# Kernel tuning notes

Hardware: AMD Instinct MI355X
Metric: run time of the kernel (lower is better)

The kernel has to match this reference:

```python
import jax, jax.numpy as jnp
import numpy as np

HIDDEN = 2560
NUM_HEADS = 80
HEAD_DIM = 64
STATE = 128
N_GROUPS = 1
CONV_K = 4
CHUNK = 256
INTER = 2 * HIDDEN                       # 5120 = NUM_HEADS * HEAD_DIM
CONV_DIM = INTER + 2 * N_GROUPS * STATE  # 5376
PROJ = INTER + CONV_DIM + NUM_HEADS      # 10576
EPS = 1e-5
DT_MIN, DT_MAX = 0.0, 100.0


def segment_sum(x):
    # x: (..., T) -> (..., T, T); out[i, j] = sum_{j < k <= i} x[k], -inf above diag
    T = x.shape[-1]
    xe = jnp.broadcast_to(x[..., :, None], x.shape + (T,))  # [i, j] = x[i]
    mask_lo = jnp.tril(jnp.ones((T, T), dtype=bool), -1)
    seg = jnp.cumsum(jnp.where(mask_lo, xe, 0.0), axis=-2)
    mask = jnp.tril(jnp.ones((T, T), dtype=bool), 0)
    return jnp.where(mask, seg, -jnp.inf)


def setup_inputs() -> dict:
    key = jax.random.key(0)
    k0, k1, k2, k3 = jax.random.split(key, 4)
    x = jax.random.normal(k0, (2, 2048, HIDDEN), jnp.float32)
    in_proj_w = jax.random.normal(k1, (PROJ, HIDDEN), jnp.float32) * (HIDDEN ** -0.5)
    conv1d_w = jax.random.normal(k2, (CONV_DIM, CONV_K), jnp.float32) * (CONV_K ** -0.5)
    conv1d_b = jnp.zeros((CONV_DIM,), jnp.float32)
    A_log = jnp.log(jnp.arange(1, NUM_HEADS + 1, dtype=jnp.float32))
    D = jnp.ones((NUM_HEADS,), jnp.float32)
    dt_bias = jnp.ones((NUM_HEADS,), jnp.float32)
    norm_weight = jnp.ones((INTER,), jnp.float32)
    out_proj_w = jax.random.normal(k3, (HIDDEN, INTER), jnp.float32) * (INTER ** -0.5)
    return dict(input_states=x, in_proj_w=in_proj_w, conv1d_w=conv1d_w,
                conv1d_b=conv1d_b, A_log=A_log, D=D, dt_bias=dt_bias,
                norm_weight=norm_weight, out_proj_w=out_proj_w)


def _mamba2_forward(input_states, in_proj_w, conv1d_w, conv1d_b, A_log, D,
                    dt_bias, norm_weight, out_proj_w):
    b, s, _ = input_states.shape
    proj = input_states @ in_proj_w.T                       # (b, s, PROJ)
    gate, hs, dt = jnp.split(proj, [INTER, INTER + CONV_DIM], axis=-1)

    # causal depthwise conv1d + SiLU
    xT = jnp.transpose(hs, (0, 2, 1))                       # (b, conv_dim, s)
    xT = jnp.pad(xT, ((0, 0), (0, 0), (CONV_K - 1, 0)))
    conv = jax.lax.conv_general_dilated(
        xT, conv1d_w[:, None, :], (1,), 'VALID',
        feature_group_count=CONV_DIM, dimension_numbers=('NCH', 'OIH', 'NCH'))
    hs = jax.nn.silu(jnp.transpose(conv + conv1d_b[None, :, None], (0, 2, 1)))

    hs, B, C = jnp.split(hs, [INTER, INTER + N_GROUPS * STATE], axis=-1)
    A = -jnp.exp(A_log)                                     # (h,)
    dt = jnp.clip(jax.nn.softplus(dt + dt_bias), DT_MIN, DT_MAX)  # (b, s, h)

    X = hs.reshape(b, s, NUM_HEADS, HEAD_DIM)
    rep = NUM_HEADS // N_GROUPS
    B = jnp.repeat(B.reshape(b, s, N_GROUPS, STATE), rep, axis=2)
    C = jnp.repeat(C.reshape(b, s, N_GROUPS, STATE), rep, axis=2)

    pad = (-s) % CHUNK
    D_res = D[None, None, :, None] * jnp.pad(X, ((0, 0), (0, pad), (0, 0), (0, 0)))
    Xd = X * dt[..., None]                                  # discretized input
    dA = A[None, None, :] * dt                              # (b, s, h)

    def chunk(t):
        t = jnp.pad(t, [(0, 0), (0, pad)] + [(0, 0)] * (t.ndim - 2))
        return t.reshape(t.shape[0], -1, CHUNK, *t.shape[2:])

    Xc, Bc, Cc = chunk(Xd), chunk(B), chunk(C)              # (b, c, l, h, ...)
    Ac = jnp.transpose(chunk(dA), (0, 3, 1, 2))             # (b, h, c, l)
    A_cum = jnp.cumsum(Ac, axis=-1)

    # 1. intra-chunk (diagonal block) outputs
    L = jnp.exp(segment_sum(Ac))                            # (b, h, c, l, l)
    G = jnp.einsum('bclhn,bcshn->bhcls', Cc, Bc)
    Y_diag = jnp.einsum('bhcls,bcshp->bclhp', G * L, Xc)

    # 2. per-chunk final states
    decay_states = jnp.exp(A_cum[..., -1:] - A_cum)         # (b, h, c, l)
    states = jnp.einsum('bclhn,bhcl,bclhp->bchpn', Bc, decay_states, Xc)

    # 3. inter-chunk recurrence
    A_last = A_cum[..., -1]                                 # (b, h, c)
    decay_chunk = jnp.exp(segment_sum(jnp.pad(A_last, ((0, 0), (0, 0), (1, 0)))))
    states = jnp.concatenate([jnp.zeros_like(states[:, :1]), states], axis=1)
    new_states = jnp.einsum('bhzc,bchpn->bzhpn', decay_chunk, states)
    states = new_states[:, :-1]                             # (b, c, h, p, n)

    # 4. state -> output conversion
    Y_off = jnp.einsum('bclhn,bchpn,bhcl->bclhp', Cc, states, jnp.exp(A_cum))

    y = (Y_diag + Y_off).reshape(b, -1, NUM_HEADS, HEAD_DIM) + D_res
    y = y[:, :s].reshape(b, s, INTER)

    # gated RMSNorm
    y = y * jax.nn.silu(gate)
    var = jnp.mean(y * y, axis=-1, keepdims=True)
    y = y * jax.lax.rsqrt(var + EPS) * norm_weight
    return y @ out_proj_w.T


def reference(input_states, in_proj_w, conv1d_w, conv1d_b, A_log, D, dt_bias,
              norm_weight, out_proj_w):
    return _mamba2_forward(input_states, in_proj_w, conv1d_w, conv1d_b, A_log,
                           D, dt_bias, norm_weight, out_proj_w)
```

## Files before the change

kernel.cpp:

```cpp
#include <hip/hip_runtime.h>
#include <hip/hip_bf16.h>
#include <math.h>

#define HIDDEN   2560
#define NUM_HEADS 80
#define HEAD_DIM 64
#define STATE    128
#define CONV_K   4
#define CHUNK    256
#define INTER    (2*HIDDEN)
#define CONV_DIM (INTER + 2*STATE)
#define PROJ     (INTER + CONV_DIM + NUM_HEADS)
#define PROJ_PAD 10624
#define NBC      336
#define EPS      1e-5f

#define BATCH 2
#define SEQ   2048
#define TOK   (BATCH*SEQ)
#define NC    (SEQ/CHUNK)
#define KSPLIT 16
#define KCH   (HIDDEN/KSPLIT)

typedef __attribute__((ext_vector_type(8))) short bf16x8;
typedef __attribute__((ext_vector_type(4))) float f32x4;

#define MFMA16(a,b,c) __builtin_amdgcn_mfma_f32_16x16x32_bf16((a),(b),(c),0,0,0)

__device__ __forceinline__ unsigned short f2bf(float f){
    union{float f;unsigned u;}v; v.f=f;
    unsigned r = v.u + 0x7fffu + ((v.u>>16)&1u);
    return (unsigned short)(r>>16);
}
__device__ __forceinline__ float bf2f(unsigned short s){
    union{unsigned u;float f;}v; v.u = ((unsigned)s)<<16; return v.f;
}
__device__ __forceinline__ void unpack8(uint4 u, float* e){
    e[0]=bf2f((unsigned short)(u.x&0xffff)); e[1]=bf2f((unsigned short)(u.x>>16));
    e[2]=bf2f((unsigned short)(u.y&0xffff)); e[3]=bf2f((unsigned short)(u.y>>16));
    e[4]=bf2f((unsigned short)(u.z&0xffff)); e[5]=bf2f((unsigned short)(u.z>>16));
    e[6]=bf2f((unsigned short)(u.w&0xffff)); e[7]=bf2f((unsigned short)(u.w>>16));
}

__device__ __forceinline__ void gld16(const void* g, void* l){
    __builtin_amdgcn_global_load_lds((const __attribute__((address_space(1))) void*)g,
                                     (__attribute__((address_space(3))) void*)l, 16, 0, 0);
}

template<bool BF16OUT>
__global__ __launch_bounds__(256) void gemm_bf16(const unsigned short* __restrict__ A, int lda,
                                                 const unsigned short* __restrict__ B, int ldb,
                                                 void* __restrict__ Cv, int ldc, int K) {
    __shared__ unsigned short As[128][64];
    __shared__ unsigned short Bs[128][64];
    int tid = threadIdx.x;
    int lane = tid & 63, wid = tid >> 6;
    int wr = wid >> 1, wc = wid & 1;

    int bm, bn;
    if ((gridDim.y & 7) == 0) {
        int bid   = blockIdx.y * gridDim.x + blockIdx.x;
        int xcd   = bid & 7;
        int local = bid >> 3;
        int mrows = gridDim.y >> 3;
        bm = (xcd * mrows + (local % mrows)) * 128;
        bn = (local / mrows) * 128;
    } else {
        bm = blockIdx.y * 128;
        bn = blockIdx.x * 128;
    }

    f32x4 acc[4][4];
    #pragma unroll
    for (int i=0;i<4;i++)
        #pragma unroll
        for (int j=0;j<4;j++) acc[i][j] = (f32x4){0.f,0.f,0.f,0.f};

    int srow_off = lane >> 3;
    int sslot    = lane & 7;

    for (int k0 = 0; k0 < K; k0 += 64) {
        #pragma unroll
        for (int q=0;q<4;q++){
            int brow = (wid*4+q)*8;
            int row  = brow + srow_off;
            int sl   = sslot ^ (row & 7);
            gld16(A + (size_t)(bm + row)*lda + k0 + sl*8, &As[brow][0]);
            gld16(B + (size_t)(bn + row)*ldb + k0 + sl*8, &Bs[brow][0]);
        }
        __syncthreads();
        #pragma unroll
        for (int kk=0; kk<64; kk+=32){
            bf16x8 a[4], b[4];
            #pragma unroll
            for (int i=0;i<4;i++){
                int row = wr*64 + i*16 + (lane&15);
                int slot = ((kk>>3) + (lane>>4)) ^ (row & 7);
                a[i] = *(const bf16x8*)&As[row][slot*8];
            }
            #pragma unroll
            for (int j=0;j<4;j++){
                int row = wc*64 + j*16 + (lane&15);
                int slot = ((kk>>3) + (lane>>4)) ^ (row & 7);
                b[j] = *(const bf16x8*)&Bs[row][slot*8];
            }
            #pragma unroll
            for (int i=0;i<4;i++)
                #pragma unroll
                for (int j=0;j<4;j++)
                    acc[i][j] = MFMA16(a[i], b[j], acc[i][j]);
        }
        __syncthreads();
    }
    #pragma unroll
    for (int i=0;i<4;i++){
        int row0 = bm + wr*64 + i*16 + (lane>>4)*4;
        #pragma unroll
        for (int j=0;j<4;j++){
            int col = bn + wc*64 + j*16 + (lane&15);
            #pragma unroll
            for (int r=0;r<4;r++){
                if (BF16OUT)
                    ((unsigned short*)Cv)[(size_t)(row0+r)*ldc + col] = f2bf(acc[i][j][r]);
                else
                    ((float*)Cv)[(size_t)(row0+r)*ldc + col] = acc[i][j][r];
            }
        }
    }
}

__global__ __launch_bounds__(256) void cvt_bf16(const float* __restrict__ in,
                                                unsigned short* __restrict__ out, size_t n4){
    size_t i4 = (size_t)blockIdx.x*256 + threadIdx.x;
    if (i4 >= n4) return;
    size_t i = i4*4;
    float4 v = *(const float4*)(in+i);
    ushort4 o; o.x=f2bf(v.x); o.y=f2bf(v.y); o.z=f2bf(v.z); o.w=f2bf(v.w);
    *(ushort4*)(out+i) = o;
}
__global__ __launch_bounds__(256) void cvt_w1(const float* __restrict__ in,
                                              unsigned short* __restrict__ out){
    size_t i4 = (size_t)blockIdx.x*256 + threadIdx.x;
    if (i4 >= (size_t)PROJ_PAD*HIDDEN/4) return;
    size_t i = i4*4;
    int row = (int)(i / HIDDEN);
    ushort4 o;
    if (row < PROJ){
        float4 v = *(const float4*)(in+i);
        o.x=f2bf(v.x); o.y=f2bf(v.y); o.z=f2bf(v.z); o.w=f2bf(v.w);
    } else { o.x=o.y=o.z=o.w=0; }
    *(ushort4*)(out+i) = o;
}

#define BM 128
#define BN 128
#define BKK 16
__global__ __launch_bounds__(256) void gemm_bc_splitk(const float* __restrict__ A, int lda,
                                                      const float* __restrict__ B, int ldb,
                                                      float* __restrict__ Cpart) {
    __shared__ float As[BKK][BM];
    __shared__ float Bs[BKK][BN];
    int tid = threadIdx.x;
    int bm = blockIdx.y * BM, bn = blockIdx.x * BN;
    int z  = blockIdx.z;
    int ty = tid >> 4, tx = tid & 15;
    float acc[8][8];
    #pragma unroll
    for (int i=0;i<8;i++)
        #pragma unroll
        for (int j=0;j<8;j++) acc[i][j]=0.f;
    int lr = tid >> 1, lk = (tid & 1) * 8;
    for (int k0 = z*KCH; k0 < (z+1)*KCH; k0 += BKK) {
        #pragma unroll
        for (int u=0;u<8;u++)
            As[lk+u][lr] = A[(size_t)(bm+lr)*lda + k0 + lk + u];
        int ncol = bn + lr;
        if (ncol < NBC) {
            #pragma unroll
            for (int u=0;u<8;u++)
                Bs[lk+u][lr] = B[(size_t)ncol*ldb + k0 + lk + u];
        } else {
            #pragma unroll
            for (int u=0;u<8;u++) Bs[lk+u][lr] = 0.f;
        }
        __syncthreads();
        #pragma unroll
        for (int k=0;k<BKK;k++){
            float a[8], bb[8];
            #pragma unroll
            for (int i=0;i<8;i++) a[i] = As[k][ty*8+i];
            #pragma unroll
            for (int j=0;j<8;j++) bb[j] = Bs[k][tx*8+j];
            #pragma unroll
            for (int i=0;i<8;i++)
                #pragma unroll
                for (int j=0;j<8;j++) acc[i][j] += a[i]*bb[j];
        }
        __syncthreads();
    }
    float* Cz = Cpart + (size_t)z*TOK*NBC;
    #pragma unroll
    for (int i=0;i<8;i++){
        int m = bm + ty*8 + i;
        #pragma unroll
        for (int j=0;j<8;j++){
            int n = bn + tx*8 + j;
            if (n < NBC) Cz[(size_t)m*NBC + n] = acc[i][j];
        }
    }
}

__global__ __launch_bounds__(256) void reduce_bc(const float* __restrict__ part,
                                                 const float* __restrict__ dt_bias,
                                                 float* __restrict__ outBC,
                                                 float* __restrict__ dtbuf) {
    size_t i4 = (size_t)blockIdx.x*256 + threadIdx.x;
    if (i4 >= (size_t)TOK*NBC/4) return;
    size_t i = i4*4;
    float4 s = *(const float4*)(part + i);
    #pragma unroll
    for (int z=1; z<KSPLIT; z++){
        float4 v = *(const float4*)(part + (size_t)z*TOK*NBC + i);
        s.x += v.x; s.y += v.y; s.z += v.z; s.w += v.w;
    }
    int col = (int)(i % NBC);
    int t   = (int)(i / NBC);
    if (col < 256) {
        *(float4*)(outBC + i) = s;
    } else {
        int h = col - 256;
        float e[4] = {s.x, s.y, s.z, s.w};
        #pragma unroll
        for (int u=0;u<4;u++){
            float xv = e[u] + dt_bias[h+u];
            float sp = (xv > 20.f) ? xv : log1pf(expf(xv));
            e[u] = fminf(fmaxf(sp, 0.f), 100.f);
        }
        float4 o; o.x=e[0]; o.y=e[1]; o.z=e[2]; o.w=e[3];
        *(float4*)(dtbuf + (size_t)t*NUM_HEADS + h) = o;
    }
}

__global__ __launch_bounds__(256) void conv_xt_kernel(const unsigned short* __restrict__ projb,
                                                      const float* __restrict__ cw,
                                                      const float* __restrict__ cb,
                                                      unsigned short* __restrict__ XT) {
    int t0 = blockIdx.x * 64;
    int d0 = blockIdx.y * 64;
    int b  = t0 / SEQ;
    int s0 = t0 % SEQ;
    __shared__ unsigned short raw[68][66];
    int tid = threadIdx.x;
    for (int f = tid; f < 67*8; f += 256){
        int r = f >> 3, g = f & 7;
        int sp = s0 - 3 + r;
        uint4 v;
        if (sp >= 0) v = *(const uint4*)(projb + ((size_t)(b*SEQ+sp))*PROJ_PAD + INTER + d0 + g*8);
        else { v.x=0u; v.y=0u; v.z=0u; v.w=0u; }
        unsigned int* dst = (unsigned int*)&raw[r][g*8];
        dst[0]=v.x; dst[1]=v.y; dst[2]=v.z; dst[3]=v.w;
    }
    __syncthreads();
    int t = tid & 63, dg = tid >> 6;
    #pragma unroll
    for (int dd = 0; dd < 16; dd++){
        int d = dg*16 + dd;
        float acc = cb[d0+d];
        #pragma unroll
        for (int j=0;j<CONV_K;j++)
            acc += cw[(d0+d)*CONV_K+j] * bf2f(raw[t+j][d]);
        float val = acc/(1.f+expf(-acc));
        XT[((size_t)(b*INTER + d0 + d))*SEQ + s0 + t] = f2bf(val);
    }
}

__global__ __launch_bounds__(256) void conv_bc_kernel(const float* __restrict__ projBC,
                                                      const float* __restrict__ cw,
                                                      const float* __restrict__ cb,
                                                      float* __restrict__ xBC_BC,
                                                      unsigned short* __restrict__ BT) {
    int idx = blockIdx.x*256 + threadIdx.x;
    if (idx >= TOK*256) return;
    int d = idx & 255;
    int t = idx >> 8;
    int b = t / SEQ, sl = t % SEQ;
    int dc = INTER + d;
    float acc = cb[dc];
    #pragma unroll
    for (int j=0;j<CONV_K;j++){
        int sp = sl - (CONV_K-1) + j;
        if (sp >= 0)
            acc += cw[dc*CONV_K+j] * projBC[((size_t)(b*SEQ+sp))*NBC + d];
    }
    float val = acc / (1.f + expf(-acc));
    xBC_BC[(size_t)t*256 + d] = val;
    if (d < 128)
        BT[((size_t)(b*128 + d))*SEQ + sl] = f2bf(val);
}

__global__ __launch_bounds__(256) void cumsum_kernel(const float* __restrict__ dtbuf,
                                                     const float* __restrict__ A_log,
                                                     float* __restrict__ A_cum) {
    int c = blockIdx.x, h = blockIdx.y, b = blockIdx.z;
    int l = threadIdx.x;
    float A = -expf(A_log[h]);
    float v = A * dtbuf[(size_t)(b*SEQ + c*CHUNK + l)*NUM_HEADS + h];
    __shared__ float buf[CHUNK];
    buf[l] = v;
    __syncthreads();
    for (int off=1; off<CHUNK; off<<=1){
        float t = (l>=off) ? buf[l-off] : 0.f;
        __syncthreads();
        buf[l] += t;
        __syncthreads();
    }
    A_cum[((size_t)b*NUM_HEADS + h)*SEQ + c*CHUNK + l] = buf[l];
}

__global__ __launch_bounds__(256) void g_kernel(const float* __restrict__ xBC_BC,
                                                unsigned short* __restrict__ G) {
    int p = blockIdx.x, c = blockIdx.y, b = blockIdx.z;
    int lt = 0, a0 = 0;
    while (a0 + lt + 1 <= p) { a0 += lt + 1; lt++; }
    int st = p - a0;
    int l0 = lt*64, s0 = st*64;
    __shared__ float Cs[64][68];
    __shared__ float Bs[64][68];
    int tid = threadIdx.x, ty = tid >> 4, tx = tid & 15;
    float acc[4][4];
    #pragma unroll
    for (int i=0;i<4;i++)
        #pragma unroll
        for (int j=0;j<4;j++) acc[i][j]=0.f;

    size_t rowC = ((size_t)(b*SEQ + c*CHUNK + l0))*256 + 128;
    size_t rowB = ((size_t)(b*SEQ + c*CHUNK + s0))*256;
    for (int kc=0; kc<2; kc++){
        #pragma unroll
        for (int it=0; it<4; it++){
            int f = tid + it*256;
            int r = f >> 4, c4 = f & 15;
            float4 cv = *(const float4*)(xBC_BC + rowC + (size_t)r*256 + kc*64 + c4*4);
            float4 bv = *(const float4*)(xBC_BC + rowB + (size_t)r*256 + kc*64 + c4*4);
            *(float4*)&Cs[r][c4*4] = cv;
            *(float4*)&Bs[r][c4*4] = bv;
        }
        __syncthreads();
        #pragma unroll 8
        for (int k=0;k<64;k++){
            float a[4], bb[4];
            #pragma unroll
            for (int i=0;i<4;i++) a[i] = Cs[ty*4+i][k];
            #pragma unroll
            for (int j=0;j<4;j++) bb[j] = Bs[tx*4+j][k];
            #pragma unroll
            for (int i=0;i<4;i++)
                #pragma unroll
                for (int j=0;j<4;j++) acc[i][j] += a[i]*bb[j];
        }
        __syncthreads();
    }
    size_t Gb = ((size_t)(b*NC + c)) << 16;
    #pragma unroll
    for (int i=0;i<4;i++){
        ushort4 g4;
        g4.x = f2bf(acc[i][0]); g4.y = f2bf(acc[i][1]);
        g4.z = f2bf(acc[i][2]); g4.w = f2bf(acc[i][3]);
        *(ushort4*)(G + Gb + (size_t)(l0 + ty*4 + i)*256 + s0 + tx*4) = g4;
    }
}

__global__ __launch_bounds__(256) void states_mfma(const unsigned short* __restrict__ XT,
                                                   const unsigned short* __restrict__ BT,
                                                   const float* __restrict__ dtbuf,
                                                   const float* __restrict__ A_cum,
                                                   float* __restrict__ statesT) {
    int c = blockIdx.x, h = blockIdx.y, b = blockIdx.z;
    __shared__ unsigned short Asx[64][64];
    __shared__ unsigned short Bsw[128][64];
    __shared__ float wl[CHUNK];
    int tid = threadIdx.x, lane = tid & 63, wid = tid >> 6;
    {
        const float* ac = A_cum + ((size_t)(b*NUM_HEADS+h))*SEQ + c*CHUNK;
        float Alast = ac[CHUNK-1];
        wl[tid] = expf(Alast - ac[tid]) * dtbuf[((size_t)(b*SEQ + c*CHUNK + tid))*NUM_HEADS + h];
    }
    __syncthreads();
    f32x4 acc[4][2];
    #pragma unroll
    for (int i=0;i<4;i++)
        #pragma unroll
        for (int j=0;j<2;j++) acc[i][j] = (f32x4){0.f,0.f,0.f,0.f};

    for (int kc = 0; kc < 4; kc++){
        int lbase = kc*64;
        #pragma unroll
        for (int q=0;q<2;q++){
            int brow = (wid*2+q)*8;
            int row  = brow + (lane>>3);
            int sl   = (lane&7) ^ (row & 7);
            gld16(XT + ((size_t)(b*INTER + h*HEAD_DIM + row))*SEQ + c*CHUNK + lbase + sl*8,
                  &Asx[brow][0]);
        }
        #pragma unroll
        for (int it=0; it<4; it++){
            int f = tid + it*256;
            int r = f >> 3, g = f & 7;
            uint4 v = *(const uint4*)(BT + ((size_t)(b*128 + r))*SEQ + c*CHUNK + lbase + g*8);
            float e[8]; unpack8(v, e);
            unsigned short o[8];
            #pragma unroll
            for (int u=0;u<8;u++) o[u] = f2bf(e[u] * wl[lbase + g*8 + u]);
            int slot = g ^ (r & 7);
            *(ushort4*)&Bsw[r][slot*8]   = *(ushort4*)&o[0];
            *(ushort4*)&Bsw[r][slot*8+4] = *(ushort4*)&o[4];
        }
        __syncthreads();
        #pragma unroll
        for (int kk=0; kk<64; kk+=32){
            bf16x8 a[4], bb[2];
            #pragma unroll
            for (int i=0;i<4;i++){
                int row = i*16 + (lane&15);
                int slot = ((kk>>3)+(lane>>4)) ^ (row&7);
                a[i] = *(const bf16x8*)&Asx[row][slot*8];
            }
            #pragma unroll
            for (int j=0;j<2;j++){
                int row = wid*32 + j*16 + (lane&15);
                int slot = ((kk>>3)+(lane>>4)) ^ (row&7);
                bb[j] = *(const bf16x8*)&Bsw[row][slot*8];
            }
            #pragma unroll
            for (int i=0;i<4;i++)
                #pragma unroll
                for (int j=0;j<2;j++)
                    acc[i][j] = MFMA16(a[i], bb[j], acc[i][j]);
        }
        __syncthreads();
    }
    size_t sb = ((size_t)((b*NC + c)*NUM_HEADS + h))*(HEAD_DIM*STATE);
    #pragma unroll
    for (int i=0;i<4;i++){
        #pragma unroll
        for (int j=0;j<2;j++){
            int n = wid*32 + j*16 + (lane&15);
            int p0 = i*16 + (lane>>4)*4;
            #pragma unroll
            for (int r=0;r<4;r++)
                statesT[sb + (size_t)(p0+r)*128 + n] = acc[i][j][r];
        }
    }
}

__global__ __launch_bounds__(256) void recur_kernel(const float* __restrict__ A_cum,
                                                    float* __restrict__ states) {
    int h = blockIdx.x, b = blockIdx.y;
    int tid = threadIdx.x;
    float Srun[32];
    #pragma unroll
    for (int i=0;i<32;i++) Srun[i]=0.f;
    const float* acum = A_cum + ((size_t)b*NUM_HEADS + h)*SEQ;
    for (int c=0;c<NC;c++){
        float alast = acum[c*CHUNK + CHUNK-1];
        float dec = expf(alast);
        size_t base = ((size_t)((b*NC + c)*NUM_HEADS + h))*(HEAD_DIM*STATE);
        #pragma unroll
        for (int i=0;i<32;i++){
            size_t idx = base + (size_t)tid + (size_t)i*256;
            float raw = states[idx];
            states[idx] = Srun[i];
            Srun[i] = Srun[i]*dec + raw;
        }
    }
}

__global__ __launch_bounds__(256) void yscan_mfma(const unsigned short* __restrict__ G,
                                                  const float* __restrict__ xBC_BC,
                                                  const unsigned short* __restrict__ XT,
                                                  const float* __restrict__ dtbuf,
                                                  const float* __restrict__ A_cum,
                                                  const float* __restrict__ statesT,
                                                  const float* __restrict__ Dvec,
                                                  unsigned short* __restrict__ projb) {
    int xb = blockIdx.x;
    int c = xb >> 2, lt = xb & 3;
    int h = blockIdx.y, b = blockIdx.z;
    int l0 = lt*64;
    __shared__ __align__(16) char pool[32768];
    unsigned short (*Cs)[128] = (unsigned short(*)[128])pool;
    unsigned short (*St)[128] = (unsigned short(*)[128])(pool + 16384);
    unsigned short (*Gw)[64]  = (unsigned short(*)[64])pool;
    unsigned short (*Xs)[64]  = (unsigned short(*)[64])(pool + 8192);
    float (*Ot)[68]           = (float(*)[68])pool;
    __shared__ float ac[CHUNK], dts[CHUNK];
    int tid = threadIdx.x, lane = tid & 63, wid = tid >> 6;
    ac[tid]  = A_cum[((size_t)(b*NUM_HEADS + h))*SEQ + c*CHUNK + tid];
    dts[tid] = dtbuf[((size_t)(b*SEQ + c*CHUNK + tid))*NUM_HEADS + h];
    __syncthreads();

    size_t stb = ((size_t)((b*NC + c)*NUM_HEADS + h))*(HEAD_DIM*STATE);
    #pragma unroll
    for (int it=0; it<8; it++){
        int f = tid + it*256;
        int r = f >> 5, c4 = f & 31;
        float4 v = *(const float4*)(xBC_BC + ((size_t)(b*SEQ + c*CHUNK + l0 + r))*256 + 128 + c4*4);
        unsigned short o[4] = {f2bf(v.x),f2bf(v.y),f2bf(v.z),f2bf(v.w)};
        int col = c4*4;
        int slot = (col>>3) ^ (r&7);
        *(ushort4*)&Cs[r][slot*8 + (col&7)] = *(ushort4*)o;
        float4 w = *(const float4*)(statesT + stb + (size_t)r*128 + c4*4);
        unsigned short o2[4] = {f2bf(w.x),f2bf(w.y),f2bf(w.z),f2bf(w.w)};
        *(ushort4*)&St[r][slot*8 + (col&7)] = *(ushort4*)o2;
    }
    __syncthreads();

    f32x4 acc1[4];
    #pragma unroll
    for (int j=0;j<4;j++) acc1[j] = (f32x4){0.f,0.f,0.f,0.f};
    #pragma unroll
    for (int kk=0; kk<128; kk+=32){
        int arow = wid*16 + (lane&15);
        int aslot = ((kk>>3)+(lane>>4)) ^ (arow&7);
        bf16x8 a = *(const bf16x8*)&Cs[arow][aslot*8];
        #pragma unroll
        for (int j=0;j<4;j++){
            int brow = j*16 + (lane&15);
            int bslot = ((kk>>3)+(lane>>4)) ^ (brow&7);
            bf16x8 bb = *(const bf16x8*)&St[brow][bslot*8];
            acc1[j] = MFMA16(a, bb, acc1[j]);
        }
    }
    float el[4];
    #pragma unroll
    for (int r=0;r<4;r++) el[r] = expf(ac[l0 + wid*16 + (lane>>4)*4 + r]);
    float master[4][4];
    #pragma unroll
    for (int j=0;j<4;j++)
        #pragma unroll
        for (int r=0;r<4;r++) master[j][r] = acc1[j][r]*el[r];
    __syncthreads();

    size_t Gb = ((size_t)(b*NC + c)) << 16;
    f32x4 acc2[4];
    #pragma unroll
    for (int j=0;j<4;j++) acc2[j] = (f32x4){0.f,0.f,0.f,0.f};
    for (int st=0; st<=lt; st++){
        int s0 = st*64;
        #pragma unroll
        for (int it=0; it<2; it++){
            int f = tid + it*256;
            int r = f >> 3, g = f & 7;
            uint4 v = *(const uint4*)(G + Gb + (size_t)(l0 + r)*256 + s0 + g*8);
            float e[8]; unpack8(v, e);
            float acl = ac[l0 + r];
            unsigned short o[8];
            #pragma unroll
            for (int u=0;u<8;u++){
                int s = s0 + g*8 + u;
                float w = (s <= l0 + r) ? expf(acl - ac[s])*dts[s] : 0.f;
                o[u] = f2bf(e[u]*w);
            }
            int slot = g ^ (r&7);
            *(ushort4*)&Gw[r][slot*8]   = *(ushort4*)&o[0];
            *(ushort4*)&Gw[r][slot*8+4] = *(ushort4*)&o[4];
        }
        #pragma unroll
        for (int q=0;q<2;q++){
            int brow = (wid*2+q)*8;
            int row  = brow + (lane>>3);
            int sl   = (lane&7) ^ (row&7);
            gld16(XT + ((size_t)(b*INTER + h*HEAD_DIM + row))*SEQ + c*CHUNK + s0 + sl*8,
                  &Xs[brow][0]);
        }
        __syncthreads();
        #pragma unroll
        for (int kk=0; kk<64; kk+=32){
            int arow = wid*16 + (lane&15);
            int aslot = ((kk>>3)+(lane>>4)) ^ (arow&7);
            bf16x8 a = *(const bf16x8*)&Gw[arow][aslot*8];
            #pragma unroll
            for (int j=0;j<4;j++){
                int brow = j*16 + (lane&15);
                int bslot = ((kk>>3)+(lane>>4)) ^ (brow&7);
                bf16x8 bb = *(const bf16x8*)&Xs[brow][bslot*8];
                acc2[j] = MFMA16(a, bb, acc2[j]);
            }
        }
        if (st < lt) __syncthreads();
    }

    float Dh = Dvec[h];
    #pragma unroll
    for (int j=0;j<4;j++){
        int p = j*16 + (lane&15);
        #pragma unroll
        for (int r=0;r<4;r++){
            int sl_ = wid*16 + (lane>>4)*4 + r;
            int slot = (sl_>>3) ^ (p&7);
            float xv = bf2f(Xs[p][slot*8 + (sl_&7)]);
            master[j][r] += acc2[j][r] + Dh*xv;
        }
    }
    __syncthreads();

    #pragma unroll
    for (int j=0;j<4;j++){
        int p = j*16 + (lane&15);
        #pragma unroll
        for (int r=0;r<4;r++)
            Ot[wid*16 + (lane>>4)*4 + r][p] = master[j][r];
    }
    __syncthreads();
    #pragma unroll
    for (int it=0; it<4; it++){
        int f = tid + it*256;
        int r = f >> 4, c4 = f & 15;
        ushort4 o;
        o.x = f2bf(Ot[r][c4*4+0]); o.y = f2bf(Ot[r][c4*4+1]);
        o.z = f2bf(Ot[r][c4*4+2]); o.w = f2bf(Ot[r][c4*4+3]);
        *(ushort4*)(projb + ((size_t)(b*SEQ + c*CHUNK + l0 + r))*PROJ_PAD + INTER + h*HEAD_DIM + c4*4) = o;
    }
}

__global__ __launch_bounds__(256) void gate_norm_kernel(const unsigned short* __restrict__ projb,
                                                        const float* __restrict__ normw,
                                                        unsigned short* __restrict__ yb) {
    int t = blockIdx.x;
    int tid = threadIdx.x;
    const unsigned short* row = projb + (size_t)t*PROJ_PAD;
    __shared__ float red[4];
    float vals[20];
    float ss = 0.f;
    #pragma unroll
    for (int i=0;i<5;i++){
        int j = (tid + i*256)*4;
        ushort4 g4 = *(const ushort4*)(row + j);
        ushort4 y4 = *(const ushort4*)(row + INTER + j);
        #pragma unroll
        for (int u=0;u<4;u++){
            float g = bf2f(((const unsigned short*)&g4)[u]);
            float y = bf2f(((const unsigned short*)&y4)[u]);
            float gv = g / (1.f + expf(-g));
            float v = y * gv;
            vals[i*4+u] = v;
            ss += v*v;
        }
    }
    #pragma unroll
    for (int off=32; off; off>>=1) ss += __shfl_xor(ss, off);
    if ((tid&63)==0) red[tid>>6] = ss;
    __syncthreads();
    float tot = red[0]+red[1]+red[2]+red[3];
    float inv = rsqrtf(tot/(float)INTER + EPS);
    #pragma unroll
    for (int i=0;i<5;i++){
        int j = (tid + i*256)*4;
        ushort4 o;
        o.x = f2bf(vals[i*4+0] * inv * normw[j+0]);
        o.y = f2bf(vals[i*4+1] * inv * normw[j+1]);
        o.z = f2bf(vals[i*4+2] * inv * normw[j+2]);
        o.w = f2bf(vals[i*4+3] * inv * normw[j+3]);
        *(ushort4*)(yb + (size_t)t*INTER + j) = o;
    }
}

extern "C" void kernel_launch(void* const* d_in, const int* in_sizes, int n_in,
                              void* d_out, int out_size, void* d_ws, size_t ws_size,
                              hipStream_t stream) {
    const float* x        = (const float*)d_in[0];
    const float* in_w     = (const float*)d_in[1];
    const float* conv_w   = (const float*)d_in[2];
    const float* conv_b   = (const float*)d_in[3];
    const float* A_log    = (const float*)d_in[4];
    const float* Dvec     = (const float*)d_in[5];
    const float* dt_bias  = (const float*)d_in[6];
    const float* norm_w   = (const float*)d_in[7];
    const float* out_w    = (const float*)d_in[8];
    float* out = (float*)d_out;
    (void)ws_size; (void)n_in; (void)in_sizes; (void)out_size;

    const size_t PROJB   = (size_t)TOK*PROJ_PAD*2;
    const size_t PROJBCB = (size_t)TOK*NBC*4;
    const size_t XTB     = (size_t)TOK*INTER*2;
    const size_t XBCBCB  = (size_t)TOK*256*4;
    const size_t BTB     = (size_t)BATCH*128*SEQ*2;
    const size_t GBYTES  = (size_t)BATCH*NC*CHUNK*CHUNK*2;
    const size_t DTB     = (size_t)TOK*NUM_HEADS*4;
    const size_t ACUMB   = DTB;
    const size_t STB     = (size_t)BATCH*NC*NUM_HEADS*HEAD_DIM*STATE*4;
    const size_t XB      = (size_t)TOK*HIDDEN*2;
    const size_t YB      = (size_t)TOK*INTER*2;

    char* base = (char*)d_ws;
    size_t off = 0;
    unsigned short* projb  = (unsigned short*)(base + off); off += PROJB;
    float* projBC          = (float*)(base + off);          off += PROJBCB;
    unsigned short* XTp    = (unsigned short*)(base + off); off += XTB;
    float* xBC_BC          = (float*)(base + off);          off += XBCBCB;
    unsigned short* BTp    = (unsigned short*)(base + off); off += BTB;
    unsigned short* Gp     = (unsigned short*)(base + off); off += GBYTES;
    float* dtbuf           = (float*)(base + off);          off += DTB;
    float* A_cum           = (float*)(base + off);          off += ACUMB;
    float* statesT         = (float*)(base + off);          off += STB;
    char*  T               = base + off;
    unsigned short* xb  = (unsigned short*)T;
    unsigned short* w1b = (unsigned short*)(T + XB);
    float* bcpart       = (float*)T;
    unsigned short* yb  = (unsigned short*)T;
    unsigned short* w2b = (unsigned short*)(T + YB);

    const size_t XB_E = (size_t)TOK*HIDDEN;
    const size_t W1_E = (size_t)PROJ_PAD*HIDDEN;
    const size_t W2_E = (size_t)HIDDEN*INTER;

    cvt_bf16<<<(unsigned)((XB_E/4+255)/256), 256, 0, stream>>>(x, xb, XB_E/4);
    cvt_w1<<<(unsigned)((W1_E/4+255)/256), 256, 0, stream>>>(in_w, w1b);

    gemm_bf16<true><<<dim3(PROJ_PAD/128, TOK/128), 256, 0, stream>>>(xb, HIDDEN, w1b, HIDDEN,
                                                                     projb, PROJ_PAD, HIDDEN);
    gemm_bc_splitk<<<dim3((NBC+BN-1)/BN, TOK/BM, KSPLIT), 256, 0, stream>>>(
        x, HIDDEN, in_w + (size_t)(INTER+INTER)*HIDDEN, HIDDEN, bcpart);
    reduce_bc<<<(unsigned)(((size_t)TOK*NBC/4+255)/256), 256, 0, stream>>>(bcpart, dt_bias, projBC, dtbuf);

    conv_xt_kernel<<<dim3(TOK/64, INTER/64), 256, 0, stream>>>(projb, conv_w, conv_b, XTp);
    conv_bc_kernel<<<(TOK*256+255)/256, 256, 0, stream>>>(projBC, conv_w, conv_b, xBC_BC, BTp);
    cvt_bf16<<<(unsigned)((W2_E/4+255)/256), 256, 0, stream>>>(out_w, w2b, W2_E/4);
    cumsum_kernel<<<dim3(NC, NUM_HEADS, BATCH), 256, 0, stream>>>(dtbuf, A_log, A_cum);
    g_kernel<<<dim3(10, NC, BATCH), 256, 0, stream>>>(xBC_BC, Gp);
    states_mfma<<<dim3(NC, NUM_HEADS, BATCH), 256, 0, stream>>>(XTp, BTp, dtbuf, A_cum, statesT);
    recur_kernel<<<dim3(NUM_HEADS, BATCH), 256, 0, stream>>>(A_cum, statesT);
    yscan_mfma<<<dim3(NC*4, NUM_HEADS, BATCH), 256, 0, stream>>>(Gp, xBC_BC, XTp, dtbuf, A_cum,
                                                                 statesT, Dvec, projb);
    gate_norm_kernel<<<TOK, 256, 0, stream>>>(projb, norm_w, yb);
    gemm_bf16<false><<<dim3(HIDDEN/128, TOK/128), 256, 0, stream>>>(yb, INTER, w2b, INTER,
                                                                    out, HIDDEN, INTER);
}
```

Measured before the change: 874.7 us.

## Replace in-projection GEMM with 256x256-tile, 4-stage pipelined MFMA kernel

Adds a new bf16 GEMM kernel for the large in-projection that uses 256x256 output tiles, 512 threads, and a 4-deep LDS ring buffer fed by direct global-to-LDS loads with XOR-swizzled slots. It also raises instruction priority around the MFMA loop. The intent is more reuse per loaded byte and better overlap of loads with compute than the previous 128x128 kernel. PROJ_PAD grows to 10752 so the N dimension divides by 256, which adds some wasted padded columns and needs matching buffer sizes. The large accumulator tile increases register pressure.

```diff
diff --git a/kernel.cpp b/kernel.cpp
--- a/kernel.cpp
+++ b/kernel.cpp
@@ -11,7 +11,7 @@
 #define INTER    (2*HIDDEN)
 #define CONV_DIM (INTER + 2*STATE)
 #define PROJ     (INTER + CONV_DIM + NUM_HEADS)
-#define PROJ_PAD 10624
+#define PROJ_PAD 10752
 #define NBC      336
 #define EPS      1e-5f
 
@@ -45,6 +45,88 @@
 __device__ __forceinline__ void gld16(const void* g, void* l){
     __builtin_amdgcn_global_load_lds((const __attribute__((address_space(1))) void*)g,
                                      (__attribute__((address_space(3))) void*)l, 16, 0, 0);
+}
+
+__global__ __launch_bounds__(512, 2) void gemm_bf16_256(const unsigned short* __restrict__ A, int lda,
+                                                        const unsigned short* __restrict__ B, int ldb,
+                                                        unsigned short* __restrict__ C, int ldc, int K) {
+    __shared__ unsigned short LA[4][256][32];
+    __shared__ unsigned short LB[4][256][32];
+    int tid = threadIdx.x, lane = tid & 63, wid = tid >> 6;
+    int wm = wid >> 2, wn = wid & 3;
+
+    int bid   = blockIdx.y * gridDim.x + blockIdx.x;
+    int xcd   = bid & 7;
+    int local = bid >> 3;
+    int mrows = gridDim.y >> 3;
+    int bm = (xcd * mrows + (local % mrows)) * 256;
+    int bn = (local / mrows) * 256;
+
+    f32x4 acc[8][4];
+    #pragma unroll
+    for (int i=0;i<8;i++)
+        #pragma unroll
+        for (int j=0;j<4;j++) acc[i][j] = (f32x4){0.f,0.f,0.f,0.f};
+
+    int srow  = lane >> 2;
+    int sslot = lane & 3;
+    int NT = K >> 5;
+
+    #define STAGE256(t_, s_) { int k0 = (t_)*32;                                         \
+        _Pragma("unroll")                                                                \
+        for (int q=0;q<2;q++){                                                           \
+            int brow = (wid*2+q)*16;                                                     \
+            int row  = brow + srow;                                                      \
+            int sl   = sslot ^ ((row>>1)&3);                                             \
+            gld16(A + (size_t)(bm + row)*lda + k0 + sl*8, &LA[s_][brow][0]);             \
+            gld16(B + (size_t)(bn + row)*ldb + k0 + sl*8, &LB[s_][brow][0]);             \
+        } }
+
+    STAGE256(0, 0);
+    STAGE256(1, 1);
+    STAGE256(2, 2);
+    asm volatile("s_waitcnt vmcnt(8)" ::: "memory");
+    __builtin_amdgcn_s_barrier();
+
+    for (int t = 0; t < NT; ++t) {
+        int slot = t & 3;
+        if (t + 3 < NT) STAGE256(t+3, (t+3)&3);
+        bf16x8 bfr[4];
+        #pragma unroll
+        for (int j=0;j<4;j++){
+            int row = wn*64 + j*16 + (lane&15);
+            int sl  = (lane>>4) ^ ((row>>1)&3);
+            bfr[j] = *(const bf16x8*)&LB[slot][row][sl*8];
+        }
+        __builtin_amdgcn_s_setprio(1);
+        #pragma unroll
+        for (int i=0;i<8;i++){
+            int row = wm*128 + i*16 + (lane&15);
+            int sl  = (lane>>4) ^ ((row>>1)&3);
+            bf16x8 afr = *(const bf16x8*)&LA[slot][row][sl*8];
+            #pragma unroll
+            for (int j=0;j<4;j++)
+                acc[i][j] = MFMA16(afr, bfr[j], acc[i][j]);
+        }
+        __builtin_amdgcn_s_setprio(0);
+        if (t < NT-3)       asm volatile("s_waitcnt vmcnt(8)" ::: "memory");
+        else if (t == NT-3) asm volatile("s_waitcnt vmcnt(4)" ::: "memory");
+        else                asm volatile("s_waitcnt vmcnt(0)" ::: "memory");
+        __builtin_amdgcn_s_barrier();
+    }
+    #undef STAGE256
+
+    #pragma unroll
+    for (int i=0;i<8;i++){
+        int row0 = bm + wm*128 + i*16 + (lane>>4)*4;
+        #pragma unroll
+        for (int j=0;j<4;j++){
+            int col = bn + wn*64 + j*16 + (lane&15);
+            #pragma unroll
+            for (int r=0;r<4;r++)
+                C[(size_t)(row0+r)*ldc + col] = f2bf(acc[i][j][r]);
+        }
+    }
 }
 
 template<bool BF16OUT>
@@ -717,8 +799,8 @@
     cvt_bf16<<<(unsigned)((XB_E/4+255)/256), 256, 0, stream>>>(x, xb, XB_E/4);
     cvt_w1<<<(unsigned)((W1_E/4+255)/256), 256, 0, stream>>>(in_w, w1b);
 
-    gemm_bf16<true><<<dim3(PROJ_PAD/128, TOK/128), 256, 0, stream>>>(xb, HIDDEN, w1b, HIDDEN,
-                                                                     projb, PROJ_PAD, HIDDEN);
+    gemm_bf16_256<<<dim3(PROJ_PAD/256, TOK/256), 512, 0, stream>>>(xb, HIDDEN, w1b, HIDDEN,
+                                                                   projb, PROJ_PAD, HIDDEN);
     gemm_bc_splitk<<<dim3((NBC+BN-1)/BN, TOK/BM, KSPLIT), 256, 0, stream>>>(
         x, HIDDEN, in_w + (size_t)(INTER+INTER)*HIDDEN, HIDDEN, bcpart);
     reduce_bc<<<(unsigned)(((size_t)TOK*NBC/4+255)/256), 256, 0, stream>>>(bcpart, dt_bias, projBC, dtbuf);
```

New measurement: 927.6 us. 6.1% more time.

## Replace FP32 B/C/dt split-K GEMM with split-bf16 MFMA and fuse prep/conv kernels

Applied to the files above, without the earlier changes.

Swaps the scalar FP32 split-K GEMM for the B, C and dt projection columns for an MFMA kernel. It keeps near-FP32 accuracy by splitting x and the weights into bf16 hi/lo parts and accumulating three products. It also halves the split-K factor, pads the output to 384 columns, merges the x/weight conversions into one prep kernel, and merges the two conv kernels into one launch. The aim is to remove the slow CUDA-core FP32 GEMM and cut launch count, at the cost of extra hi/lo conversion traffic and three MFMA passes.

```diff
diff --git a/kernel.cpp b/kernel.cpp
--- a/kernel.cpp
+++ b/kernel.cpp
@@ -13,14 +13,15 @@
 #define PROJ     (INTER + CONV_DIM + NUM_HEADS)
 #define PROJ_PAD 10624
 #define NBC      336
+#define NBCP     384
 #define EPS      1e-5f
 
 #define BATCH 2
 #define SEQ   2048
 #define TOK   (BATCH*SEQ)
 #define NC    (SEQ/CHUNK)
-#define KSPLIT 16
-#define KCH   (HIDDEN/KSPLIT)
+#define KSPL2 8
+#define KCH2  (HIDDEN/KSPL2)
 
 typedef __attribute__((ext_vector_type(8))) short bf16x8;
 typedef __attribute__((ext_vector_type(4))) float f32x4;
@@ -129,6 +130,169 @@
     }
 }
 
+__global__ __launch_bounds__(256) void bc_splitk_mfma(const unsigned short* __restrict__ xhi,
+                                                      const unsigned short* __restrict__ xlo,
+                                                      const unsigned short* __restrict__ whi,
+                                                      const unsigned short* __restrict__ wlo,
+                                                      float* __restrict__ Cpart) {
+    __shared__ unsigned short As[128][64];
+    __shared__ unsigned short Bs[128][64];
+    int tid = threadIdx.x;
+    int lane = tid & 63, wid = tid >> 6;
+    int wr = wid >> 1, wc = wid & 1;
+    int bn = blockIdx.x * 128, bm = blockIdx.y * 128, z = blockIdx.z;
+
+    f32x4 acc[4][4];
+    #pragma unroll
+    for (int i=0;i<4;i++)
+        #pragma unroll
+        for (int j=0;j<4;j++) acc[i][j] = (f32x4){0.f,0.f,0.f,0.f};
+
+    int srow_off = lane >> 3;
+    int sslot    = lane & 7;
+
+    for (int term = 0; term < 3; ++term){
+        const unsigned short* A = (term==2) ? xlo : xhi;
+        const unsigned short* B = (term==0) ? wlo : whi;
+        for (int k0 = z*KCH2; k0 < z*KCH2 + KCH2; k0 += 64) {
+            #pragma unroll
+            for (int q=0;q<4;q++){
+                int brow = (wid*4+q)*8;
+                int row  = brow + srow_off;
+                int sl   = sslot ^ (row & 7);
+                gld16(A + (size_t)(bm + row)*HIDDEN + k0 + sl*8, &As[brow][0]);
+                gld16(B + (size_t)(bn + row)*HIDDEN + k0 + sl*8, &Bs[brow][0]);
+            }
+            __syncthreads();
+            #pragma unroll
+            for (int kk=0; kk<64; kk+=32){
+                bf16x8 a[4], b[4];
+                #pragma unroll
+                for (int i=0;i<4;i++){
+                    int row = wr*64 + i*16 + (lane&15);
+                    int slot = ((kk>>3) + (lane>>4)) ^ (row & 7);
+                    a[i] = *(const bf16x8*)&As[row][slot*8];
+                }
+                #pragma unroll
+                for (int j=0;j<4;j++){
+                    int row = wc*64 + j*16 + (lane&15);
+                    int slot = ((kk>>3) + (lane>>4)) ^ (row & 7);
+                    b[j] = *(const bf16x8*)&Bs[row][slot*8];
+                }
+                #pragma unroll
+                for (int i=0;i<4;i++)
+                    #pragma unroll
+                    for (int j=0;j<4;j++)
+                        acc[i][j] = MFMA16(a[i], b[j], acc[i][j]);
+            }
+            __syncthreads();
+        }
+    }
+    float* Cz = Cpart + (size_t)z*TOK*NBCP;
+    #pragma unroll
+    for (int i=0;i<4;i++){
+        int row0 = bm + wr*64 + i*16 + (lane>>4)*4;
+        #pragma unroll
+        for (int j=0;j<4;j++){
+            int col = bn + wc*64 + j*16 + (lane&15);
+            #pragma unroll
+            for (int r=0;r<4;r++)
+                Cz[(size_t)(row0+r)*NBCP + col] = acc[i][j][r];
+        }
+    }
+}
+
+__global__ __launch_bounds__(256) void reduce_bc2(const float* __restrict__ part,
+                                                  const float* __restrict__ dt_bias,
+                                                  float* __restrict__ outBC,
+                                                  float* __restrict__ dtbuf) {
+    size_t i4 = (size_t)blockIdx.x*256 + threadIdx.x;
+    if (i4 >= (size_t)TOK*NBCP/4) return;
+    size_t i = i4*4;
+    float4 s = *(const float4*)(part + i);
+    #pragma unroll
+    for (int z=1; z<KSPL2; z++){
+        float4 v = *(const float4*)(part + (size_t)z*TOK*NBCP + i);
+        s.x += v.x; s.y += v.y; s.z += v.z; s.w += v.w;
+    }
+    int col = (int)(i % NBCP);
+    int t   = (int)(i / NBCP);
+    if (col < 256) {
+        *(float4*)(outBC + (size_t)t*NBC + col) = s;
+    } else if (col < NBC) {
+        int h = col - 256;
+        float e[4] = {s.x, s.y, s.z, s.w};
+        #pragma unroll
+        for (int u=0;u<4;u++){
+            float xv = e[u] + dt_bias[h+u];
+            float sp = (xv > 20.f) ? xv : log1pf(expf(xv));
+            e[u] = fminf(fmaxf(sp, 0.f), 100.f);
+        }
+        float4 o; o.x=e[0]; o.y=e[1]; o.z=e[2]; o.w=e[3];
+        *(float4*)(dtbuf + (size_t)t*NUM_HEADS + h) = o;
+    }
+}
+
+#define N4A ((size_t)TOK*HIDDEN/4)
+#define N4B ((size_t)PROJ_PAD*HIDDEN/4)
+#define N4C ((size_t)NBCP*HIDDEN/4)
+__global__ __launch_bounds__(256) void prep_kernel(const float* __restrict__ x,
+                                                   const float* __restrict__ in_w,
+                                                   unsigned short* __restrict__ xhi,
+                                                   unsigned short* __restrict__ xlo,
+                                                   unsigned short* __restrict__ w1b,
+                                                   unsigned short* __restrict__ wbc_hi,
+                                                   unsigned short* __restrict__ wbc_lo) {
+    size_t gid = (size_t)blockIdx.x*256 + threadIdx.x;
+    if (gid < N4A) {
+        size_t i = gid*4;
+        float4 v = *(const float4*)(x + i);
+        float e[4] = {v.x, v.y, v.z, v.w};
+        ushort4 h, l;
+        unsigned short* hp = (unsigned short*)&h;
+        unsigned short* lp = (unsigned short*)&l;
+        #pragma unroll
+        for (int u=0;u<4;u++){
+            unsigned short hv = f2bf(e[u]);
+            hp[u] = hv;
+            lp[u] = f2bf(e[u] - bf2f(hv));
+        }
+        *(ushort4*)(xhi + i) = h;
+        *(ushort4*)(xlo + i) = l;
+    } else if (gid < N4A + N4B) {
+        size_t j = gid - N4A;
+        size_t i = j*4;
+        int row = (int)(i / HIDDEN);
+        ushort4 o;
+        if (row < PROJ){
+            float4 v = *(const float4*)(in_w + i);
+            o.x=f2bf(v.x); o.y=f2bf(v.y); o.z=f2bf(v.z); o.w=f2bf(v.w);
+        } else { o.x=o.y=o.z=o.w=0; }
+        *(ushort4*)(w1b + i) = o;
+    } else {
+        size_t j = gid - N4A - N4B;
+        size_t i = j*4;
+        int row = (int)(i / HIDDEN);
+        int kk  = (int)(i % HIDDEN);
+        ushort4 h, l;
+        h.x=h.y=h.z=h.w=0; l.x=l.y=l.z=l.w=0;
+        if (row < NBC){
+            float4 v = *(const float4*)(in_w + (size_t)(2*INTER + row)*HIDDEN + kk);
+            float e[4] = {v.x, v.y, v.z, v.w};
+            unsigned short* hp = (unsigned short*)&h;
+            unsigned short* lp = (unsigned short*)&l;
+            #pragma unroll
+            for (int u=0;u<4;u++){
+                unsigned short hv = f2bf(e[u]);
+                hp[u] = hv;
+                lp[u] = f2bf(e[u] - bf2f(hv));
+            }
+        }
+        *(ushort4*)(wbc_hi + i) = h;
+        *(ushort4*)(wbc_lo + i) = l;
+    }
+}
+
 __global__ __launch_bounds__(256) void cvt_bf16(const float* __restrict__ in,
                                                 unsigned short* __restrict__ out, size_t n4){
     size_t i4 = (size_t)blockIdx.x*256 + threadIdx.x;
@@ -138,164 +302,62 @@
     ushort4 o; o.x=f2bf(v.x); o.y=f2bf(v.y); o.z=f2bf(v.z); o.w=f2bf(v.w);
     *(ushort4*)(out+i) = o;
 }
-__global__ __launch_bounds__(256) void cvt_w1(const float* __restrict__ in,
-                                              unsigned short* __restrict__ out){
-    size_t i4 = (size_t)blockIdx.x*256 + threadIdx.x;
-    if (i4 >= (size_t)PROJ_PAD*HIDDEN/4) return;
-    size_t i = i4*4;
-    int row = (int)(i / HIDDEN);
-    ushort4 o;
-    if (row < PROJ){
-        float4 v = *(const float4*)(in+i);
-        o.x=f2bf(v.x); o.y=f2bf(v.y); o.z=f2bf(v.z); o.w=f2bf(v.w);
-    } else { o.x=o.y=o.z=o.w=0; }
-    *(ushort4*)(out+i) = o;
-}
-
-#define BM 128
-#define BN 128
-#define BKK 16
-__global__ __launch_bounds__(256) void gemm_bc_splitk(const float* __restrict__ A, int lda,
-                                                      const float* __restrict__ B, int ldb,
-                                                      float* __restrict__ Cpart) {
-    __shared__ float As[BKK][BM];
-    __shared__ float Bs[BKK][BN];
+
+__global__ __launch_bounds__(256) void conv_fused(const unsigned short* __restrict__ projb,
+                                                  const float* __restrict__ projBC,
+                                                  const float* __restrict__ cw,
+                                                  const float* __restrict__ cb,
+                                                  unsigned short* __restrict__ XT,
+                                                  float* __restrict__ xBC_BC,
+                                                  unsigned short* __restrict__ BT) {
+    __shared__ unsigned short raw[68][66];
+    int bid = blockIdx.x;
     int tid = threadIdx.x;
-    int bm = blockIdx.y * BM, bn = blockIdx.x * BN;
-    int z  = blockIdx.z;
-    int ty = tid >> 4, tx = tid & 15;
-    float acc[8][8];
-    #pragma unroll
-    for (int i=0;i<8;i++)
-        #pragma unroll
-        for (int j=0;j<8;j++) acc[i][j]=0.f;
-    int lr = tid >> 1, lk = (tid & 1) * 8;
-    for (int k0 = z*KCH; k0 < (z+1)*KCH; k0 += BKK) {
-        #pragma unroll
-        for (int u=0;u<8;u++)
-            As[lk+u][lr] = A[(size_t)(bm+lr)*lda + k0 + lk + u];
-        int ncol = bn + lr;
-        if (ncol < NBC) {
-            #pragma unroll
-            for (int u=0;u<8;u++)
-                Bs[lk+u][lr] = B[(size_t)ncol*ldb + k0 + lk + u];
-        } else {
-            #pragma unroll
-            for (int u=0;u<8;u++) Bs[lk+u][lr] = 0.f;
-        }
-        __syncthreads();
-        #pragma unroll
-        for (int k=0;k<BKK;k++){
-            float a[8], bb[8];
-            #pragma unroll
-            for (int i=0;i<8;i++) a[i] = As[k][ty*8+i];
-            #pragma unroll
-            for (int j=0;j<8;j++) bb[j] = Bs[k][tx*8+j];
-            #pragma unroll
-            for (int i=0;i<8;i++)
-                #pragma unroll
-                for (int j=0;j<8;j++) acc[i][j] += a[i]*bb[j];
-        }
-        __syncthreads();
-    }
-    float* Cz = Cpart + (size_t)z*TOK*NBC;
-    #pragma unroll
-    for (int i=0;i<8;i++){
-        int m = bm + ty*8 + i;
-        #pragma unroll
-        for (int j=0;j<8;j++){
-            int n = bn + tx*8 + j;
-            if (n < NBC) Cz[(size_t)m*NBC + n] = acc[i][j];
-        }
-    }
-}
-
-__global__ __launch_bounds__(256) void reduce_bc(const float* __restrict__ part,
-                                                 const float* __restrict__ dt_bias,
-                                                 float* __restrict__ outBC,
-                                                 float* __restrict__ dtbuf) {
-    size_t i4 = (size_t)blockIdx.x*256 + threadIdx.x;
-    if (i4 >= (size_t)TOK*NBC/4) return;
-    size_t i = i4*4;
-    float4 s = *(const float4*)(part + i);
-    #pragma unroll
-    for (int z=1; z<KSPLIT; z++){
-        float4 v = *(const float4*)(part + (size_t)z*TOK*NBC + i);
-        s.x += v.x; s.y += v.y; s.z += v.z; s.w += v.w;
-    }
-    int col = (int)(i % NBC);
-    int t   = (int)(i / NBC);
-    if (col < 256) {
-        *(float4*)(outBC + i) = s;
+    if (bid < (TOK/64)*(INTER/64)) {
+        int bx = bid & 63, by = bid >> 6;
+        int t0 = bx * 64, d0 = by * 64;
+        int b  = t0 / SEQ;
+        int s0 = t0 % SEQ;
+        for (int f = tid; f < 67*8; f += 256){
+            int r = f >> 3, g = f & 7;
+            int sp = s0 - 3 + r;
+            uint4 v;
+            if (sp >= 0) v = *(const uint4*)(projb + ((size_t)(b*SEQ+sp))*PROJ_PAD + INTER + d0 + g*8);
+            else { v.x=0u; v.y=0u; v.z=0u; v.w=0u; }
+            unsigned int* dst = (unsigned int*)&raw[r][g*8];
+            dst[0]=v.x; dst[1]=v.y; dst[2]=v.z; dst[3]=v.w;
+        }
+        __syncthreads();
+        int t = tid & 63, dg = tid >> 6;
+        #pragma unroll
+        for (int dd = 0; dd < 16; dd++){
+            int d = dg*16 + dd;
+            float acc = cb[d0+d];
+            #pragma unroll
+            for (int j=0;j<CONV_K;j++)
+                acc += cw[(d0+d)*CONV_K+j] * bf2f(raw[t+j][d]);
+            float val = acc/(1.f+expf(-acc));
+            XT[((size_t)(b*INTER + d0 + d))*SEQ + s0 + t] = f2bf(val);
+        }
     } else {
-        int h = col - 256;
-        float e[4] = {s.x, s.y, s.z, s.w};
-        #pragma unroll
-        for (int u=0;u<4;u++){
-            float xv = e[u] + dt_bias[h+u];
-            float sp = (xv > 20.f) ? xv : log1pf(expf(xv));
-            e[u] = fminf(fmaxf(sp, 0.f), 100.f);
-        }
-        float4 o; o.x=e[0]; o.y=e[1]; o.z=e[2]; o.w=e[3];
-        *(float4*)(dtbuf + (size_t)t*NUM_HEADS + h) = o;
-    }
-}
-
-__global__ __launch_bounds__(256) void conv_xt_kernel(const unsigned short* __restrict__ projb,
-                                                      const float* __restrict__ cw,
-                                                      const float* __restrict__ cb,
-                                                      unsigned short* __restrict__ XT) {
-    int t0 = blockIdx.x * 64;
-    int d0 = blockIdx.y * 64;
-    int b  = t0 / SEQ;
-    int s0 = t0 % SEQ;
-    __shared__ unsigned short raw[68][66];
-    int tid = threadIdx.x;
-    for (int f = tid; f < 67*8; f += 256){
-        int r = f >> 3, g = f & 7;
-        int sp = s0 - 3 + r;
-        uint4 v;
-        if (sp >= 0) v = *(const uint4*)(projb + ((size_t)(b*SEQ+sp))*PROJ_PAD + INTER + d0 + g*8);
-        else { v.x=0u; v.y=0u; v.z=0u; v.w=0u; }
-        unsigned int* dst = (unsigned int*)&raw[r][g*8];
-        dst[0]=v.x; dst[1]=v.y; dst[2]=v.z; dst[3]=v.w;
-    }
-    __syncthreads();
-    int t = tid & 63, dg = tid >> 6;
-    #pragma unroll
-    for (int dd = 0; dd < 16; dd++){
-        int d = dg*16 + dd;
-        float acc = cb[d0+d];
-        #pragma unroll
-        for (int j=0;j<CONV_K;j++)
-            acc += cw[(d0+d)*CONV_K+j] * bf2f(raw[t+j][d]);
-        float val = acc/(1.f+expf(-acc));
-        XT[((size_t)(b*INTER + d0 + d))*SEQ + s0 + t] = f2bf(val);
-    }
-}
-
-__global__ __launch_bounds__(256) void conv_bc_kernel(const float* __restrict__ projBC,
-                                                      const float* __restrict__ cw,
-                                                      const float* __restrict__ cb,
-                                                      float* __restrict__ xBC_BC,
-                                                      unsigned short* __restrict__ BT) {
-    int idx = blockIdx.x*256 + threadIdx.x;
-    if (idx >= TOK*256) return;
-    int d = idx & 255;
-    int t = idx >> 8;
-    int b = t / SEQ, sl = t % SEQ;
-    int dc = INTER + d;
-    float acc = cb[dc];
-    #pragma unroll
-    for (int j=0;j<CONV_K;j++){
-        int sp = sl - (CONV_K-1) + j;
-        if (sp >= 0)
-            acc += cw[dc*CONV_K+j] * projBC[((size_t)(b*SEQ+sp))*NBC + d];
-    }
-    float val = acc / (1.f + expf(-acc));
-    xBC_BC[(size_t)t*256 + d] = val;
-    if (d < 128)
-        BT[((size_t)(b*128 + d))*SEQ + sl] = f2bf(val);
+        int idx = (bid - (TOK/64)*(INTER/64))*256 + tid;
+        if (idx >= TOK*256) return;
+        int d = idx & 255;
+        int t = idx >> 8;
+        int b = t / SEQ, sl = t % SEQ;
+        int dc = INTER + d;
+        float acc = cb[dc];
+        #pragma unroll
+        for (int j=0;j<CONV_K;j++){
+            int sp = sl - (CONV_K-1) + j;
+            if (sp >= 0)
+                acc += cw[dc*CONV_K+j] * projBC[((size_t)(b*SEQ+sp))*NBC + d];
+        }
+        float val = acc / (1.f + expf(-acc));
+        xBC_BC[(size_t)t*256 + d] = val;
+        if (d < 128)
+            BT[((size_t)(b*128 + d))*SEQ + sl] = f2bf(val);
+    }
 }
 
 __global__ __launch_bounds__(256) void cumsum_kernel(const float* __restrict__ dtbuf,
@@ -689,8 +751,9 @@
     const size_t DTB     = (size_t)TOK*NUM_HEADS*4;
     const size_t ACUMB   = DTB;
     const size_t STB     = (size_t)BATCH*NC*NUM_HEADS*HEAD_DIM*STATE*4;
-    const size_t XB      = (size_t)TOK*HIDDEN*2;
-    const size_t YB      = (size_t)TOK*INTER*2;
+    const size_t XHB   = (size_t)TOK*HIDDEN*2;
+    const size_t WBCB  = (size_t)NBCP*HIDDEN*2;
+    const size_t YBB   = (size_t)TOK*INTER*2;
 
     char* base = (char*)d_ws;
     size_t off = 0;
@@ -704,27 +767,27 @@
     float* A_cum           = (float*)(base + off);          off += ACUMB;
     float* statesT         = (float*)(base + off);          off += STB;
     char*  T               = base + off;
-    unsigned short* xb  = (unsigned short*)T;
-    unsigned short* w1b = (unsigned short*)(T + XB);
-    float* bcpart       = (float*)T;
-    unsigned short* yb  = (unsigned short*)T;
-    unsigned short* w2b = (unsigned short*)(T + YB);
-
-    const size_t XB_E = (size_t)TOK*HIDDEN;
-    const size_t W1_E = (size_t)PROJ_PAD*HIDDEN;
+    unsigned short* xhi    = (unsigned short*)T;
+    unsigned short* xlo    = (unsigned short*)(T + XHB);
+    unsigned short* wbc_hi = (unsigned short*)(T + 2*XHB);
+    unsigned short* wbc_lo = (unsigned short*)(T + 2*XHB + WBCB);
+    unsigned short* w1b    = (unsigned short*)(T + 2*XHB + 2*WBCB);
+    float* bcpart          = (float*)w1b;
+    unsigned short* yb     = (unsigned short*)T;
+    unsigned short* w2b    = (unsigned short*)(T + YBB);
+
     const size_t W2_E = (size_t)HIDDEN*INTER;
 
-    cvt_bf16<<<(unsigned)((XB_E/4+255)/256), 256, 0, stream>>>(x, xb, XB_E/4);
-    cvt_w1<<<(unsigned)((W1_E/4+255)/256), 256, 0, stream>>>(in_w, w1b);
-
-    gemm_bf16<true><<<dim3(PROJ_PAD/128, TOK/128), 256, 0, stream>>>(xb, HIDDEN, w1b, HIDDEN,
+    {
+        unsigned total_blocks = (unsigned)((N4A + N4B + N4C) / 256);
+        prep_kernel<<<total_blocks, 256, 0, stream>>>(x, in_w, xhi, xlo, w1b, wbc_hi, wbc_lo);
+    }
+    gemm_bf16<true><<<dim3(PROJ_PAD/128, TOK/128), 256, 0, stream>>>(xhi, HIDDEN, w1b, HIDDEN,
                                                                      projb, PROJ_PAD, HIDDEN);
-    gemm_bc_splitk<<<dim3((NBC+BN-1)/BN, TOK/BM, KSPLIT), 256, 0, stream>>>(
-        x, HIDDEN, in_w + (size_t)(INTER+INTER)*HIDDEN, HIDDEN, bcpart);
-    reduce_bc<<<(unsigned)(((size_t)TOK*NBC/4+255)/256), 256, 0, stream>>>(bcpart, dt_bias, projBC, dtbuf);
-
-    conv_xt_kernel<<<dim3(TOK/64, INTER/64), 256, 0, stream>>>(projb, conv_w, conv_b, XTp);
-    conv_bc_kernel<<<(TOK*256+255)/256, 256, 0, stream>>>(projBC, conv_w, conv_b, xBC_BC, BTp);
+    bc_splitk_mfma<<<dim3(NBCP/128, TOK/128, KSPL2), 256, 0, stream>>>(xhi, xlo, wbc_hi, wbc_lo, bcpart);
+    reduce_bc2<<<(unsigned)(((size_t)TOK*NBCP/4)/256), 256, 0, stream>>>(bcpart, dt_bias, projBC, dtbuf);
+    conv_fused<<<(TOK/64)*(INTER/64) + TOK, 256, 0, stream>>>(projb, projBC, conv_w, conv_b,
+                                                              XTp, xBC_BC, BTp);
     cvt_bf16<<<(unsigned)((W2_E/4+255)/256), 256, 0, stream>>>(out_w, w2b, W2_E/4);
     cumsum_kernel<<<dim3(NC, NUM_HEADS, BATCH), 256, 0, stream>>>(dtbuf, A_log, A_cum);
     g_kernel<<<dim3(10, NC, BATCH), 256, 0, stream>>>(xBC_BC, Gp);
```

Measured after the change: 765.7 us. -12.5%, faster.
